# Performance work log

Measured on AMD Instinct MI355X. Metric: run time of the kernel, lower is better.

Reference implementation:

```python
import jax, jax.numpy as jnp
import numpy as np

N_NODES = 100000
N_REL = 4
N_EDGES = 400000
IN_F, H_F, OUT_F = 128, 128, 64


def setup_inputs() -> dict:
    key = jax.random.key(0)
    ks = jax.random.split(key, 7)
    x = jax.random.normal(ks[0], (N_NODES, IN_F), dtype=jnp.float32)
    src_idx = jax.random.randint(ks[1], (N_REL, N_EDGES), 0, N_NODES, dtype=jnp.int64)
    dst_idx = jax.random.randint(ks[2], (N_REL, N_EDGES), 0, N_NODES, dtype=jnp.int64)
    # Glorot-ish scale for the per-relation GraphConv weights
    W1 = jax.random.normal(ks[3], (N_REL, IN_F, H_F), dtype=jnp.float32) * (1.0 / np.sqrt(IN_F))
    b1 = jnp.zeros((N_REL, H_F), dtype=jnp.float32)
    W2 = jax.random.normal(ks[4], (N_REL, H_F, OUT_F), dtype=jnp.float32) * (1.0 / np.sqrt(H_F))
    b2 = jnp.zeros((N_REL, OUT_F), dtype=jnp.float32)
    return {"x": x, "src_idx": src_idx, "dst_idx": dst_idx,
            "W1": W1, "b1": b1, "W2": W2, "b2": b2}


def _graph_conv(x, src, dst, W, b):
    """DGL GraphConv with norm='both': out = D_in^{-1/2} A^T D_out^{-1/2} x W + b."""
    n = x.shape[0]
    ones = jnp.ones(src.shape[0], dtype=x.dtype)
    deg_out = jnp.maximum(jax.ops.segment_sum(ones, src, num_segments=n), 1.0)
    deg_in = jnp.maximum(jax.ops.segment_sum(ones, dst, num_segments=n), 1.0)
    xn = x * jax.lax.rsqrt(deg_out)[:, None]              # [N, F] src-side norm
    msg = jnp.take(xn, src, axis=0)                        # [E, F] gather
    agg = jax.ops.segment_sum(msg, dst, num_segments=n)   # [N, F] scatter-add
    agg = agg * jax.lax.rsqrt(deg_in)[:, None]            # dst-side norm
    return agg @ W + b


def _hetero_layer(x, src_idx, dst_idx, Ws, bs):
    # per-relation conv, sum-aggregated across relations (HeteroGraphConv 'sum')
    per_rel = jax.vmap(lambda s, d, W, b: _graph_conv(x, s, d, W, b))(src_idx, dst_idx, Ws, bs)
    return per_rel.sum(axis=0)


def reference(x, src_idx, dst_idx, W1, b1, W2, b2):
    h = jax.nn.relu(_hetero_layer(x, src_idx, dst_idx, W1, b1))
    return _hetero_layer(h, src_idx, dst_idx, W2, b2)
```

## Files before the change

kernel.cpp:

```cpp
#include <hip/hip_runtime.h>
#include <hip/hip_bf16.h>

#define NN 100000
#define NR 4
#define NE 400000
#define INF 128
#define HF 128
#define OUTF 64

#define WIN 16384
#define WIN2 (WIN / 2)
#define NWIN 7
#define SUB 16
#define SLICE (NE / SUB)

#define GB 782

#define NBKT 256
#define BKTW 391
#define CAPB 16
#define CAP2 12288
#define EPB 2048
#define SPR 196
#define S1B (NR * SPR)
#define FGRID (GB + S1B)

typedef __attribute__((ext_vector_type(8))) short s16x8;
typedef __attribute__((ext_vector_type(4))) float f32x4;

__global__ __launch_bounds__(256) void deg_win_kernel(const int* __restrict__ src,
                                                      const int* __restrict__ dst,
                                                      unsigned int* __restrict__ parts) {
    __shared__ unsigned int hist[WIN2];
    int arr = blockIdx.z;
    int r   = blockIdx.y;
    int win = blockIdx.x / SUB;
    int sub = blockIdx.x % SUB;
    const int4* idx4 = (const int4*)((arr ? dst : src) + (size_t)r * NE + (size_t)sub * SLICE);
    int base = win * WIN;

    uint4 z4 = make_uint4(0, 0, 0, 0);
    for (int i = threadIdx.x; i < WIN2 / 4; i += 256) ((uint4*)hist)[i] = z4;
    __syncthreads();

    auto proc = [&](int4 v) {
        int a;
        a = v.x - base; if ((unsigned)a < WIN) atomicAdd(&hist[a >> 1], 1u << ((a & 1) << 4));
        a = v.y - base; if ((unsigned)a < WIN) atomicAdd(&hist[a >> 1], 1u << ((a & 1) << 4));
        a = v.z - base; if ((unsigned)a < WIN) atomicAdd(&hist[a >> 1], 1u << ((a & 1) << 4));
        a = v.w - base; if ((unsigned)a < WIN) atomicAdd(&hist[a >> 1], 1u << ((a & 1) << 4));
    };

    constexpr int NV = SLICE / 4;
    int i = threadIdx.x;
    for (; i + 256 < NV; i += 512) {
        int4 va = idx4[i];
        int4 vb = idx4[i + 256];
        proc(va);
        proc(vb);
    }
    if (i < NV) proc(idx4[i]);
    __syncthreads();

    unsigned int* outp = parts + ((((size_t)arr * NR + r) * NWIN + win) * SUB + sub) * WIN2;
    for (int j = threadIdx.x; j < WIN2 / 4; j += 256)
        ((uint4*)outp)[j] = ((const uint4*)hist)[j];
}

__global__ void red_norm_kernel(const unsigned int* __restrict__ parts, int* __restrict__ deg_tot,
                                float* __restrict__ rno, float* __restrict__ rni) {
    int n = blockIdx.x * blockDim.x + threadIdx.x;
    if (n >= NN) return;
    if (n == 0) deg_tot[NN] = 0;
    int win = n / WIN, off = n % WIN;
    int word = off >> 1, sh = (off & 1) << 4;
    int tot = 0;
    #pragma unroll
    for (int r = 0; r < NR; r++) {
        const unsigned int* p0 = parts + (((size_t)0 * NR + r) * NWIN + win) * SUB * WIN2 + word;
        const unsigned int* p1 = parts + (((size_t)1 * NR + r) * NWIN + win) * SUB * WIN2 + word;
        int so = 0, si = 0;
        #pragma unroll
        for (int s = 0; s < SUB; s++) {
            so += (p0[(size_t)s * WIN2] >> sh) & 0xFFFFu;
            si += (p1[(size_t)s * WIN2] >> sh) & 0xFFFFu;
        }
        rno[(size_t)r * NN + n] = rsqrtf(fmaxf((float)so, 1.0f));
        rni[(size_t)r * NN + n] = rsqrtf(fmaxf((float)si, 1.0f));
        tot += si;
    }
    deg_tot[n] = tot;
}

__global__ void scan_block_kernel(const int* __restrict__ in, int* __restrict__ out,
                                  int* __restrict__ blockSums, int n) {
    __shared__ int sd[256];
    int t = threadIdx.x;
    int base = blockIdx.x * 1024 + t * 4;
    int v[4];
    #pragma unroll
    for (int j = 0; j < 4; j++) v[j] = (base + j < n) ? ((in[base + j] + 7) & ~7) : 0;
    int ts = v[0] + v[1] + v[2] + v[3];
    sd[t] = ts;
    __syncthreads();
    int acc = ts;
    for (int off = 1; off < 256; off <<= 1) {
        int x = (t >= off) ? sd[t - off] : 0;
        __syncthreads();
        acc += x; sd[t] = acc;
        __syncthreads();
    }
    int run = acc - ts;
    #pragma unroll
    for (int j = 0; j < 4; j++) {
        if (base + j < n) out[base + j] = run;
        run += v[j];
    }
    if (t == 255) blockSums[blockIdx.x] = acc;
}

__global__ void scan_sums_kernel(int* __restrict__ blockSums, int nb) {
    __shared__ int sd[512];
    int t = threadIdx.x;
    int v = (t < nb) ? blockSums[t] : 0;
    sd[t] = v;
    __syncthreads();
    int acc = v;
    for (int off = 1; off < 512; off <<= 1) {
        int x = (t >= off) ? sd[t - off] : 0;
        __syncthreads();
        acc += x; sd[t] = acc;
        __syncthreads();
    }
    if (t < nb) blockSums[t] = acc - v;
}

__global__ void scan_add_kernel(int* __restrict__ row_ptr, const int* __restrict__ blockSums,
                                int* __restrict__ ovfcnt, int n) {
    int i = blockIdx.x * blockDim.x + threadIdx.x;
    if (i < n) row_ptr[i] = row_ptr[i] + blockSums[i >> 10];
    if (i == 0) ovfcnt[0] = 0;
}

__global__ void prep_kernel(const float* __restrict__ W1, const float* __restrict__ W2,
                            const float* __restrict__ b1, const float* __restrict__ b2,
                            __hip_bfloat16* __restrict__ Wt1, __hip_bfloat16* __restrict__ Wt2,
                            float* __restrict__ bsum1, float* __restrict__ bsum2) {
    if (blockIdx.x == 384) {
        int t = threadIdx.x;
        if (t < HF) {
            float s = 0.f;
            for (int r = 0; r < NR; r++) s += b1[r * HF + t];
            bsum1[t] = s;
        } else if (t < HF + OUTF) {
            int f = t - HF;
            float s = 0.f;
            for (int r = 0; r < NR; r++) s += b2[r * OUTF + f];
            bsum2[f] = s;
        }
        return;
    }
    int id = blockIdx.x * 256 + threadIdx.x;
    if (id < NR * HF * INF) {
        int r = id >> 14, rem = id & 16383;
        int n_ = rem >> 7, k = rem & 127;
        Wt1[id] = __float2bfloat16(W1[((size_t)r * INF + k) * HF + n_]);
    } else {
        int id2 = id - NR * HF * INF;
        if (id2 < NR * OUTF * HF) {
            int r = id2 >> 13, rem = id2 & 8191;
            int n_ = rem >> 7, k = rem & 127;
            Wt2[id2] = __float2bfloat16(W2[((size_t)r * HF + k) * OUTF + n_]);
        }
    }
}

__device__ __forceinline__ s16x8 pack_bf16x8(float4 a0, float4 a1) {
    union { s16x8 v; __hip_bfloat162 h[4]; } u;
    u.h[0] = __float22bfloat162_rn(make_float2(a0.x, a0.y));
    u.h[1] = __float22bfloat162_rn(make_float2(a0.z, a0.w));
    u.h[2] = __float22bfloat162_rn(make_float2(a1.x, a1.y));
    u.h[3] = __float22bfloat162_rn(make_float2(a1.z, a1.w));
    return u.v;
}

__device__ __forceinline__ void load_lds_16(const void* g, void* l) {
    __builtin_amdgcn_global_load_lds(
        (const __attribute__((address_space(1))) void*)g,
        (__attribute__((address_space(3))) void*)l, 16, 0, 0);
}

template<int F, typename AT>
__device__ __forceinline__ void gemm_body(int mbase, const AT* __restrict__ Xb,
                                          const __hip_bfloat16* __restrict__ Wt,
                                          __hip_bfloat16* __restrict__ Zb, int nrel,
                                          __hip_bfloat16* Bs) {
    constexpr int NT = F / 16;
    constexpr int NG = F * 16;

    int tid  = threadIdx.x;
    int wid  = tid >> 6;
    int lane = tid & 63;
    int quad = lane >> 4;
    int l16  = lane & 15;
    int sw   = l16 & 7;

    int bofs[4];
    #pragma unroll
    for (int kb = 0; kb < 4; kb++)
        bofs[kb] = l16 * 256 + (((kb * 4 + quad) ^ sw) << 4);

    s16x8 afr[2][4];
    #pragma unroll
    for (int mt = 0; mt < 2; mt++) {
        int mrow = mbase + mt * 64 + wid * 16 + l16;
        if (mrow >= NN) mrow = NN - 1;
        #pragma unroll
        for (int kb = 0; kb < 4; kb++) {
            if constexpr (sizeof(AT) == 4) {
                const float* xr = (const float*)Xb + (size_t)mrow * 128 + kb * 32 + quad * 8;
                float4 a0 = *(const float4*)xr;
                float4 a1 = *(const float4*)(xr + 4);
                afr[mt][kb] = pack_bf16x8(a0, a1);
            } else {
                afr[mt][kb] = *(const s16x8*)((const __hip_bfloat16*)Xb + (size_t)mrow * 128 + kb * 32 + quad * 8);
            }
        }
    }

    for (int rel = 0; rel < nrel; rel++) {
        if (rel) __syncthreads();

        {
            const char* W = (const char*)(Wt + (size_t)rel * F * 128);
            #pragma unroll
            for (int it = 0; it < NG / 256; it++) {
                int dg = it * 256 + tid;
                int sg = dg ^ ((dg >> 4) & 7);
                load_lds_16(W + (size_t)sg * 16, (char*)Bs + (size_t)(dg & ~63) * 16);
            }
        }
        __syncthreads();

        __hip_bfloat16* Z = Zb + (size_t)rel * NN * F;

        f32x4 acc[2][NT];
        #pragma unroll
        for (int nt = 0; nt < NT; nt++) {
            acc[0][nt] = (f32x4){0.f, 0.f, 0.f, 0.f};
            acc[1][nt] = (f32x4){0.f, 0.f, 0.f, 0.f};
            #pragma unroll
            for (int kb = 0; kb < 4; kb++) {
                s16x8 bfr = *(const s16x8*)((const char*)Bs + nt * 4096 + bofs[kb]);
                acc[0][nt] = __builtin_amdgcn_mfma_f32_16x16x32_bf16(bfr, afr[0][kb], acc[0][nt], 0, 0, 0);
                acc[1][nt] = __builtin_amdgcn_mfma_f32_16x16x32_bf16(bfr, afr[1][kb], acc[1][nt], 0, 0, 0);
            }
        }

        #pragma unroll
        for (int mt = 0; mt < 2; mt++) {
            int g = mbase + mt * 64 + wid * 16 + l16;
            if (g < NN) {
                #pragma unroll
                for (int nt = 0; nt < NT; nt++) {
                    union { uint2 u; __hip_bfloat162 h[2]; } o;
                    o.h[0] = __float22bfloat162_rn(make_float2(acc[mt][nt][0], acc[mt][nt][1]));
                    o.h[1] = __float22bfloat162_rn(make_float2(acc[mt][nt][2], acc[mt][nt][3]));
                    *(uint2*)(Z + (size_t)g * F + nt * 16 + quad * 4) = o.u;
                }
            }
        }
    }
}

__global__ __launch_bounds__(256, 3) void fusedC_kernel(
        const float* __restrict__ x, const __hip_bfloat16* __restrict__ Wt1,
        __hip_bfloat16* __restrict__ Zb,
        const int* __restrict__ src, const int* __restrict__ dst,
        unsigned int* __restrict__ temp, unsigned char* __restrict__ cnt,
        int* __restrict__ ovfcnt, int2* __restrict__ ovf) {
    __shared__ __attribute__((aligned(16))) char sm[HF * 128 * 2];
    int b = blockIdx.x;
    int sb;
    if (b < 2 * GB) {
        if ((b & 1) == 0) {
            gemm_body<HF, float>((b >> 1) * 128, x, Wt1, Zb, NR, (__hip_bfloat16*)sm);
            return;
        }
        sb = b >> 1;
    } else sb = b - GB;

    int* cur = (int*)sm;
    int r = sb / SPR;
    int q = sb % SPR;
    int base_e = q * EPB;
    int n = NE - base_e; if (n > EPB) n = EPB;
    int tid = threadIdx.x;
    cur[tid] = 0;
    __syncthreads();

    if (tid * 8 < n) {
        const int4* sp4 = (const int4*)(src + (size_t)r * NE + base_e);
        const int4* dp4 = (const int4*)(dst + (size_t)r * NE + base_e);
        int4 s0 = sp4[tid * 2], s1 = sp4[tid * 2 + 1];
        int4 d0 = dp4[tid * 2], d1 = dp4[tid * 2 + 1];
        auto one = [&](int s, int d) {
            unsigned k = (unsigned)d / BKTW;
            int dlo = d - (int)k * BKTW;
            unsigned rec = ((unsigned)(r * NN + s) << 9) | (unsigned)dlo;
            int pos = atomicAdd(&cur[k], 1);
            if (pos < CAPB)
                temp[((size_t)sb * NBKT + k) * CAPB + pos] = rec;
            else
                ovf[atomicAdd(ovfcnt, 1)] = make_int2((int)k, (int)rec);
        };
        one(s0.x, d0.x); one(s0.y, d0.y); one(s0.z, d0.z); one(s0.w, d0.w);
        one(s1.x, d1.x); one(s1.y, d1.y); one(s1.z, d1.z); one(s1.w, d1.w);
    }
    __syncthreads();

    int c = cur[tid]; if (c > CAPB) c = CAPB;
    cnt[(size_t)sb * NBKT + tid] = (unsigned char)c;
}

__global__ __launch_bounds__(256) void pass2_kernel(const unsigned int* __restrict__ temp,
                                                    const unsigned char* __restrict__ cnt,
                                                    const int* __restrict__ ovfcnt,
                                                    const int2* __restrict__ ovf,
                                                    const int* __restrict__ row_ptr,
                                                    const float* __restrict__ rno,
                                                    const float* __restrict__ rni,
                                                    int2* __restrict__ edges) {
    __shared__ __attribute__((aligned(16))) int2 stg[CAP2];
    __shared__ int cur[BKTW + 1];
    int k   = blockIdx.x;
    int D0  = k * BKTW;
    int ND  = NN - D0; if (ND > BKTW) ND = BKTW;
    int base = row_ptr[D0];
    int span = row_ptr[D0 + ND] - base;
    int tid  = threadIdx.x;
    int novf = ovfcnt[0];

    if (span <= CAP2) {
        int4 z = make_int4(0, 0, 0, 0);
        for (int j = tid; j < (span >> 1); j += 256) ((int4*)stg)[j] = z;
        for (int i = tid; i < ND; i += 256) cur[i] = row_ptr[D0 + i] - base;
        __syncthreads();
        for (int j = tid; j < S1B; j += 256) {
            int c = cnt[(size_t)j * NBKT + k];
            const unsigned int* cell = temp + ((size_t)j * NBKT + k) * CAPB;
            for (int i = 0; i < c; i++) {
                unsigned rec = cell[i];
                int dlo = rec & 511;
                unsigned idx = rec >> 9;
                int p = atomicAdd(&cur[dlo], 1);
                float cf = rno[idx] * rni[(size_t)(idx / NN) * NN + D0 + dlo];
                stg[p] = make_int2((int)(idx << 8), __float_as_int(cf));
            }
        }
        for (int o = tid; o < novf; o += 256) {
            int2 e = ovf[o];
            if (e.x == k) {
                unsigned rec = (unsigned)e.y;
                int dlo = rec & 511;
                unsigned idx = rec >> 9;
                int p = atomicAdd(&cur[dlo], 1);
                float cf = rno[idx] * rni[(size_t)(idx / NN) * NN + D0 + dlo];
                stg[p] = make_int2((int)(idx << 8), __float_as_int(cf));
            }
        }
        __syncthreads();
        int4* dq = (int4*)(edges + base);
        const int4* sq = (const int4*)stg;
        for (int j = tid; j < (span >> 1); j += 256) dq[j] = sq[j];
    } else {
        int4 z = make_int4(0, 0, 0, 0);
        int4* dq = (int4*)(edges + base);
        for (int j = tid; j < (span >> 1); j += 256) dq[j] = z;
        for (int i = tid; i < ND; i += 256) cur[i] = row_ptr[D0 + i];
        __syncthreads();
        for (int j = tid; j < S1B; j += 256) {
            int c = cnt[(size_t)j * NBKT + k];
            const unsigned int* cell = temp + ((size_t)j * NBKT + k) * CAPB;
            for (int i = 0; i < c; i++) {
                unsigned rec = cell[i];
                int dlo = rec & 511;
                unsigned idx = rec >> 9;
                int p = atomicAdd(&cur[dlo], 1);
                float cf = rno[idx] * rni[(size_t)(idx / NN) * NN + D0 + dlo];
                edges[p] = make_int2((int)(idx << 8), __float_as_int(cf));
            }
        }
        for (int o = tid; o < novf; o += 256) {
            int2 e = ovf[o];
            if (e.x == k) {
                unsigned rec = (unsigned)e.y;
                int dlo = rec & 511;
                unsigned idx = rec >> 9;
                int p = atomicAdd(&cur[dlo], 1);
                float cf = rno[idx] * rni[(size_t)(idx / NN) * NN + D0 + dlo];
                edges[p] = make_int2((int)(idx << 8), __float_as_int(cf));
            }
        }
    }
}

template<int F, typename AT>
__global__ __launch_bounds__(256, 3) void gemm_all(const AT* __restrict__ Xb,
                                                   const __hip_bfloat16* __restrict__ Wt,
                                                   __hip_bfloat16* __restrict__ Zb, int nrel) {
    __shared__ __attribute__((aligned(16))) __hip_bfloat16 Bs[F * 128];
    gemm_body<F, AT>(blockIdx.x * 128, Xb, Wt, Zb, nrel, Bs);
}

template<int F, bool RELU, bool OUT_F32>
__global__ __launch_bounds__(256) void gather_merged(const int* __restrict__ row_ptr,
                              const int2* __restrict__ edges,
                              const __hip_bfloat16* __restrict__ Zb,
                              float* __restrict__ outf, __hip_bfloat16* __restrict__ outb,
                              const float* __restrict__ bsum) {
    int wid  = threadIdx.x >> 6;
    int lane = threadIdx.x & 63;
    int n = blockIdx.x * 4 + wid;
    int beg = row_ptr[n];
    int end = row_ptr[n + 1];

    if constexpr (F == 128) {
        const char* Zl = (const char*)Zb + lane * 4;
        float2 a = *(const float2*)(bsum + lane * 2);
        for (int p = beg; p < end; p += 8) {
            int2 e[8];
            #pragma unroll
            for (int j = 0; j < 8; j++) e[j] = edges[p + j];
            float2 zz[8];
            #pragma unroll
            for (int j = 0; j < 8; j++)
                zz[j] = __bfloat1622float2(*(const __hip_bfloat162*)(Zl + e[j].x));
            #pragma unroll
            for (int j = 0; j < 8; j++) {
                float c = __int_as_float(e[j].y);
                a.x = fmaf(c, zz[j].x, a.x);
                a.y = fmaf(c, zz[j].y, a.y);
            }
        }
        if constexpr (RELU) { a.x = fmaxf(a.x, 0.f); a.y = fmaxf(a.y, 0.f); }
        *(__hip_bfloat162*)(outb + (size_t)n * 128 + lane * 2) = __float22bfloat162_rn(a);
    } else {
        const char* Zl = (const char*)Zb + lane * 2;
        float a = bsum[lane];
        for (int p = beg; p < end; p += 8) {
            int2 e[8];
            #pragma unroll
            for (int j = 0; j < 8; j++) e[j] = edges[p + j];
            float zz[8];
            #pragma unroll
            for (int j = 0; j < 8; j++)
                zz[j] = __bfloat162float(*(const __hip_bfloat16*)(Zl + (e[j].x >> 1)));
            #pragma unroll
            for (int j = 0; j < 8; j++) a = fmaf(__int_as_float(e[j].y), zz[j], a);
        }
        if constexpr (RELU) a = fmaxf(a, 0.f);
        if constexpr (OUT_F32) outf[(size_t)n * 64 + lane] = a;
        else outb[(size_t)n * 64 + lane] = __float2bfloat16(a);
    }
}

extern "C" void kernel_launch(void* const* d_in, const int* in_sizes, int n_in,
                              void* d_out, int out_size, void* d_ws, size_t ws_size,
                              hipStream_t stream) {
    const float* x   = (const float*)d_in[0];
    const int*   src = (const int*)  d_in[1];
    const int*   dst = (const int*)  d_in[2];
    const float* W1  = (const float*)d_in[3];
    const float* b1  = (const float*)d_in[4];
    const float* W2  = (const float*)d_in[5];
    const float* b2  = (const float*)d_in[6];
    float* out = (float*)d_out;

    constexpr int RN = NR * NN;
    constexpr int NSC = NN + 1;
    constexpr int NB = (NSC + 1023) / 1024;

    char* p = (char*)d_ws;
    int*   deg_tot   = (int*)p;   p += ((size_t)NN + 16) * 4;
    float* rno       = (float*)p; p += (size_t)RN * 4;
    float* rni       = (float*)p; p += (size_t)RN * 4;
    int*   row_ptr   = (int*)p;   p += ((size_t)NN + 16) * 4;
    int*   cursor    = (int*)p;   p += (size_t)NN * 4;
    int*   blockSums = (int*)p;   p += 1024 * 4;
    int2*  edges     = (int2*)p;  p += ((size_t)NR * NE + 8 * NN) * 8;
    float* bsum1 = (float*)p; p += HF * 4;
    float* bsum2 = (float*)p; p += OUTF * 4;
    __hip_bfloat16* hb  = (__hip_bfloat16*)p; p += (size_t)NN * HF * 2;
    __hip_bfloat16* Wt1 = (__hip_bfloat16*)p; p += (size_t)NR * HF * INF * 2;
    __hip_bfloat16* Wt2 = (__hip_bfloat16*)p; p += (size_t)NR * OUTF * HF * 2;
    __hip_bfloat16* Zb = (__hip_bfloat16*)p; p += (size_t)NR * NN * HF * 2;
    int2* ovf = (int2*)p; p += (size_t)NR * NE * 8;
    unsigned int* parts = (unsigned int*)Zb;
    unsigned int* temp = (unsigned int*)hb;
    unsigned char* cnt = (unsigned char*)hb + (size_t)S1B * NBKT * CAPB * 4;
    int* ovfcnt = blockSums + 512;

    prep_kernel<<<385, 256, 0, stream>>>(W1, W2, b1, b2, Wt1, Wt2, bsum1, bsum2);
    deg_win_kernel<<<dim3(NWIN * SUB, NR, 2), 256, 0, stream>>>(src, dst, parts);
    red_norm_kernel<<<(NN + 255) / 256, 256, 0, stream>>>(parts, deg_tot, rno, rni);
    scan_block_kernel<<<NB, 256, 0, stream>>>(deg_tot, row_ptr, blockSums, NSC);
    scan_sums_kernel<<<1, 512, 0, stream>>>(blockSums, NB);
    scan_add_kernel<<<(NSC + 255) / 256, 256, 0, stream>>>(row_ptr, blockSums, ovfcnt, NSC);

    fusedC_kernel<<<FGRID, 256, 0, stream>>>(x, Wt1, Zb, src, dst, temp, cnt, ovfcnt, ovf);

    pass2_kernel<<<NBKT, 256, 0, stream>>>(temp, cnt, ovfcnt, ovf, row_ptr, rno, rni, edges);

    constexpr int GG = NN / 4;

    gather_merged<HF, true, false><<<GG, 256, 0, stream>>>(
        row_ptr, edges, Zb, nullptr, hb, bsum1);

    gemm_all<OUTF, __hip_bfloat16><<<GB, 256, 0, stream>>>(hb, Wt2, Zb, 4);
    gather_merged<OUTF, false, true><<<GG, 256, 0, stream>>>(
        row_ptr, edges, Zb, out, nullptr, bsum2);
}
```

Baseline: 376.6 us.

## Split fused GEMM/bucketing kernel and parallelize GEMM across relations

Un-fuses the combined GEMM plus edge-bucketing kernel into a separate pass1 kernel and a per-relation GEMM launched on a 2D grid (node tile × relation), so each block handles one relation instead of looping over four. It adds a separate kernel that converts x to bf16 once, so the GEMM reads bf16 input. This raises GEMM parallelism and occupancy (launch bounds of 4 blocks per CU), at the cost of the input A fragments being reloaded once per relation and the lost overlap between GEMM and bucketing. It also adds extra launches and an extra pass over x.

```diff
diff --git a/kernel.cpp b/kernel.cpp
--- a/kernel.cpp
+++ b/kernel.cpp
@@ -23,7 +23,6 @@
 #define EPB 2048
 #define SPR 196
 #define S1B (NR * SPR)
-#define FGRID (GB + S1B)
 
 typedef __attribute__((ext_vector_type(8))) short s16x8;
 typedef __attribute__((ext_vector_type(4))) float f32x4;
@@ -184,19 +183,27 @@
     return u.v;
 }
 
+__global__ __launch_bounds__(256) void xb_kernel(const float* __restrict__ x,
+                                                 __hip_bfloat16* __restrict__ xb) {
+    int i = blockIdx.x * 256 + threadIdx.x;
+    const float4* xp = (const float4*)x + (size_t)i * 2;
+    float4 a0 = xp[0], a1 = xp[1];
+    *(s16x8*)(xb + (size_t)i * 8) = pack_bf16x8(a0, a1);
+}
+
 __device__ __forceinline__ void load_lds_16(const void* g, void* l) {
     __builtin_amdgcn_global_load_lds(
         (const __attribute__((address_space(1))) void*)g,
         (__attribute__((address_space(3))) void*)l, 16, 0, 0);
 }
 
-template<int F, typename AT>
-__device__ __forceinline__ void gemm_body(int mbase, const AT* __restrict__ Xb,
-                                          const __hip_bfloat16* __restrict__ Wt,
-                                          __hip_bfloat16* __restrict__ Zb, int nrel,
-                                          __hip_bfloat16* Bs) {
+template<int F>
+__global__ __launch_bounds__(256, 4) void gemm_1rel(const __hip_bfloat16* __restrict__ Xb,
+                                                    const __hip_bfloat16* __restrict__ Wt,
+                                                    __hip_bfloat16* __restrict__ Zb) {
     constexpr int NT = F / 16;
     constexpr int NG = F * 16;
+    __shared__ __attribute__((aligned(16))) __hip_bfloat16 Bs[F * 128];
 
     int tid  = threadIdx.x;
     int wid  = tid >> 6;
@@ -205,6 +212,19 @@
     int l16  = lane & 15;
     int sw   = l16 & 7;
 
+    int rel   = blockIdx.y;
+    int mbase = blockIdx.x * 128;
+
+    {
+        const char* W = (const char*)(Wt + (size_t)rel * F * 128);
+        #pragma unroll
+        for (int it = 0; it < NG / 256; it++) {
+            int dg = it * 256 + tid;
+            int sg = dg ^ ((dg >> 4) & 7);
+            load_lds_16(W + (size_t)sg * 16, (char*)Bs + (size_t)(dg & ~63) * 16);
+        }
+    }
+
     int bofs[4];
     #pragma unroll
     for (int kb = 0; kb < 4; kb++)
@@ -216,81 +236,47 @@
         int mrow = mbase + mt * 64 + wid * 16 + l16;
         if (mrow >= NN) mrow = NN - 1;
         #pragma unroll
+        for (int kb = 0; kb < 4; kb++)
+            afr[mt][kb] = *(const s16x8*)(Xb + (size_t)mrow * 128 + kb * 32 + quad * 8);
+    }
+    __syncthreads();
+
+    __hip_bfloat16* Z = Zb + (size_t)rel * NN * F;
+
+    f32x4 acc[2][NT];
+    #pragma unroll
+    for (int nt = 0; nt < NT; nt++) {
+        acc[0][nt] = (f32x4){0.f, 0.f, 0.f, 0.f};
+        acc[1][nt] = (f32x4){0.f, 0.f, 0.f, 0.f};
+        #pragma unroll
         for (int kb = 0; kb < 4; kb++) {
-            if constexpr (sizeof(AT) == 4) {
-                const float* xr = (const float*)Xb + (size_t)mrow * 128 + kb * 32 + quad * 8;
-                float4 a0 = *(const float4*)xr;
-                float4 a1 = *(const float4*)(xr + 4);
-                afr[mt][kb] = pack_bf16x8(a0, a1);
-            } else {
-                afr[mt][kb] = *(const s16x8*)((const __hip_bfloat16*)Xb + (size_t)mrow * 128 + kb * 32 + quad * 8);
+            s16x8 bfr = *(const s16x8*)((const char*)Bs + nt * 4096 + bofs[kb]);
+            acc[0][nt] = __builtin_amdgcn_mfma_f32_16x16x32_bf16(bfr, afr[0][kb], acc[0][nt], 0, 0, 0);
+            acc[1][nt] = __builtin_amdgcn_mfma_f32_16x16x32_bf16(bfr, afr[1][kb], acc[1][nt], 0, 0, 0);
+        }
+    }
+
+    #pragma unroll
+    for (int mt = 0; mt < 2; mt++) {
+        int g = mbase + mt * 64 + wid * 16 + l16;
+        if (g < NN) {
+            #pragma unroll
+            for (int nt = 0; nt < NT; nt++) {
+                union { uint2 u; __hip_bfloat162 h[2]; } o;
+                o.h[0] = __float22bfloat162_rn(make_float2(acc[mt][nt][0], acc[mt][nt][1]));
+                o.h[1] = __float22bfloat162_rn(make_float2(acc[mt][nt][2], acc[mt][nt][3]));
+                *(uint2*)(Z + (size_t)g * F + nt * 16 + quad * 4) = o.u;
             }
         }
     }
-
-    for (int rel = 0; rel < nrel; rel++) {
-        if (rel) __syncthreads();
-
-        {
-            const char* W = (const char*)(Wt + (size_t)rel * F * 128);
-            #pragma unroll
-            for (int it = 0; it < NG / 256; it++) {
-                int dg = it * 256 + tid;
-                int sg = dg ^ ((dg >> 4) & 7);
-                load_lds_16(W + (size_t)sg * 16, (char*)Bs + (size_t)(dg & ~63) * 16);
-            }
-        }
-        __syncthreads();
-
-        __hip_bfloat16* Z = Zb + (size_t)rel * NN * F;
-
-        f32x4 acc[2][NT];
-        #pragma unroll
-        for (int nt = 0; nt < NT; nt++) {
-            acc[0][nt] = (f32x4){0.f, 0.f, 0.f, 0.f};
-            acc[1][nt] = (f32x4){0.f, 0.f, 0.f, 0.f};
-            #pragma unroll
-            for (int kb = 0; kb < 4; kb++) {
-                s16x8 bfr = *(const s16x8*)((const char*)Bs + nt * 4096 + bofs[kb]);
-                acc[0][nt] = __builtin_amdgcn_mfma_f32_16x16x32_bf16(bfr, afr[0][kb], acc[0][nt], 0, 0, 0);
-                acc[1][nt] = __builtin_amdgcn_mfma_f32_16x16x32_bf16(bfr, afr[1][kb], acc[1][nt], 0, 0, 0);
-            }
-        }
-
-        #pragma unroll
-        for (int mt = 0; mt < 2; mt++) {
-            int g = mbase + mt * 64 + wid * 16 + l16;
-            if (g < NN) {
-                #pragma unroll
-                for (int nt = 0; nt < NT; nt++) {
-                    union { uint2 u; __hip_bfloat162 h[2]; } o;
-                    o.h[0] = __float22bfloat162_rn(make_float2(acc[mt][nt][0], acc[mt][nt][1]));
-                    o.h[1] = __float22bfloat162_rn(make_float2(acc[mt][nt][2], acc[mt][nt][3]));
-                    *(uint2*)(Z + (size_t)g * F + nt * 16 + quad * 4) = o.u;
-                }
-            }
-        }
-    }
-}
-
-__global__ __launch_bounds__(256, 3) void fusedC_kernel(
-        const float* __restrict__ x, const __hip_bfloat16* __restrict__ Wt1,
-        __hip_bfloat16* __restrict__ Zb,
+}
+
+__global__ __launch_bounds__(256) void pass1_kernel(
         const int* __restrict__ src, const int* __restrict__ dst,
         unsigned int* __restrict__ temp, unsigned char* __restrict__ cnt,
         int* __restrict__ ovfcnt, int2* __restrict__ ovf) {
-    __shared__ __attribute__((aligned(16))) char sm[HF * 128 * 2];
-    int b = blockIdx.x;
-    int sb;
-    if (b < 2 * GB) {
-        if ((b & 1) == 0) {
-            gemm_body<HF, float>((b >> 1) * 128, x, Wt1, Zb, NR, (__hip_bfloat16*)sm);
-            return;
-        }
-        sb = b >> 1;
-    } else sb = b - GB;
-
-    int* cur = (int*)sm;
+    __shared__ int cur[NBKT];
+    int sb = blockIdx.x;
     int r = sb / SPR;
     int q = sb % SPR;
     int base_e = q * EPB;
@@ -405,14 +391,6 @@
     }
 }
 
-template<int F, typename AT>
-__global__ __launch_bounds__(256, 3) void gemm_all(const AT* __restrict__ Xb,
-                                                   const __hip_bfloat16* __restrict__ Wt,
-                                                   __hip_bfloat16* __restrict__ Zb, int nrel) {
-    __shared__ __attribute__((aligned(16))) __hip_bfloat16 Bs[F * 128];
-    gemm_body<F, AT>(blockIdx.x * 128, Xb, Wt, Zb, nrel, Bs);
-}
-
 template<int F, bool RELU, bool OUT_F32>
 __global__ __launch_bounds__(256) void gather_merged(const int* __restrict__ row_ptr,
                               const int2* __restrict__ edges,
@@ -486,11 +464,11 @@
     float* rno       = (float*)p; p += (size_t)RN * 4;
     float* rni       = (float*)p; p += (size_t)RN * 4;
     int*   row_ptr   = (int*)p;   p += ((size_t)NN + 16) * 4;
-    int*   cursor    = (int*)p;   p += (size_t)NN * 4;
     int*   blockSums = (int*)p;   p += 1024 * 4;
     int2*  edges     = (int2*)p;  p += ((size_t)NR * NE + 8 * NN) * 8;
     float* bsum1 = (float*)p; p += HF * 4;
     float* bsum2 = (float*)p; p += OUTF * 4;
+    __hip_bfloat16* xb  = (__hip_bfloat16*)p; p += (size_t)NN * INF * 2;
     __hip_bfloat16* hb  = (__hip_bfloat16*)p; p += (size_t)NN * HF * 2;
     __hip_bfloat16* Wt1 = (__hip_bfloat16*)p; p += (size_t)NR * HF * INF * 2;
     __hip_bfloat16* Wt2 = (__hip_bfloat16*)p; p += (size_t)NR * OUTF * HF * 2;
@@ -502,22 +480,23 @@
     int* ovfcnt = blockSums + 512;
 
     prep_kernel<<<385, 256, 0, stream>>>(W1, W2, b1, b2, Wt1, Wt2, bsum1, bsum2);
+    xb_kernel<<<NN * INF / 8 / 256, 256, 0, stream>>>(x, xb);
     deg_win_kernel<<<dim3(NWIN * SUB, NR, 2), 256, 0, stream>>>(src, dst, parts);
     red_norm_kernel<<<(NN + 255) / 256, 256, 0, stream>>>(parts, deg_tot, rno, rni);
     scan_block_kernel<<<NB, 256, 0, stream>>>(deg_tot, row_ptr, blockSums, NSC);
     scan_sums_kernel<<<1, 512, 0, stream>>>(blockSums, NB);
     scan_add_kernel<<<(NSC + 255) / 256, 256, 0, stream>>>(row_ptr, blockSums, ovfcnt, NSC);
 
-    fusedC_kernel<<<FGRID, 256, 0, stream>>>(x, Wt1, Zb, src, dst, temp, cnt, ovfcnt, ovf);
-
+    pass1_kernel<<<S1B, 256, 0, stream>>>(src, dst, temp, cnt, ovfcnt, ovf);
     pass2_kernel<<<NBKT, 256, 0, stream>>>(temp, cnt, ovfcnt, ovf, row_ptr, rno, rni, edges);
 
     constexpr int GG = NN / 4;
 
+    gemm_1rel<HF><<<dim3(GB, NR), 256, 0, stream>>>(xb, Wt1, Zb);
     gather_merged<HF, true, false><<<GG, 256, 0, stream>>>(
         row_ptr, edges, Zb, nullptr, hb, bsum1);
 
-    gemm_all<OUTF, __hip_bfloat16><<<GB, 256, 0, stream>>>(hb, Wt2, Zb, 4);
+    gemm_1rel<OUTF><<<dim3(GB, NR), 256, 0, stream>>>(hb, Wt2, Zb);
     gather_merged<OUTF, false, true><<<GG, 256, 0, stream>>>(
         row_ptr, edges, Zb, out, nullptr, bsum2);
 }
```

After: 378.4 us. About the same (+0.5%).
